# Optimization experiments

Hardware: AMD Instinct MI355X
Metric: run time of the kernel (lower is better)

## Reference

```python
import jax, jax.numpy as jnp
import numpy as np

D_MODEL = 1024
N_HEADS = 16
D_HEAD = 64
D_FF = 4096
WINDOW = 256
B, T = 2, 2048


def setup_inputs() -> dict:
    key = jax.random.key(0)
    ks = jax.random.split(key, 10)
    tot = N_HEADS * D_HEAD
    def w(k, shape):
        # approximate kaiming_normal_ fan_out init: std = sqrt(2/fan_out)
        fan_out = shape[0]
        return jax.random.normal(k, shape, jnp.float32) * np.sqrt(2.0 / fan_out)
    return {
        "x": jax.random.normal(ks[0], (B, T, D_MODEL), jnp.float32),
        "ln1_w": jnp.ones((D_MODEL,), jnp.float32),
        "qkv_w": w(ks[1], (3 * tot, D_MODEL)),
        "gate_w": w(ks[2], (tot, D_MODEL)),
        "out_w": w(ks[3], (D_MODEL, tot)),
        "ln2_w": jnp.ones((D_MODEL,), jnp.float32),
        "wg": w(ks[4], (D_FF, D_MODEL)),
        "wu": w(ks[5], (D_FF, D_MODEL)),
        "wo": w(ks[6], (D_MODEL, D_FF)),
    }


def _rmsnorm(x, w):
    return x * jax.lax.rsqrt(jnp.mean(x * x, axis=-1, keepdims=True) + 1e-6) * w


def _attention(x, qkv_w, gate_w, out_w):
    Bq, Tq, _ = x.shape
    tot = N_HEADS * D_HEAD
    qkv = x @ qkv_w.T  # [B,T,3*tot]
    q, k, v = jnp.split(qkv, 3, axis=-1)
    q = q.reshape(Bq, Tq, N_HEADS, D_HEAD).transpose(0, 2, 1, 3)
    k = k.reshape(Bq, Tq, N_HEADS, D_HEAD).transpose(0, 2, 1, 3)
    v = v.reshape(Bq, Tq, N_HEADS, D_HEAD).transpose(0, 2, 1, 3)
    scale = D_HEAD ** -0.5
    scores = jnp.einsum("bhqd,bhkd->bhqk", q, k) * scale
    pos = jnp.arange(Tq)
    dist = pos[:, None] - pos[None, :]
    allowed = (dist >= 0) & (dist < WINDOW)  # causal sliding window
    mask = jnp.where(allowed, 0.0, -jnp.inf).astype(scores.dtype)
    attn = jax.nn.softmax(scores + mask[None, None], axis=-1)
    out = jnp.einsum("bhqk,bhkd->bhqd", attn, v)
    out = out.transpose(0, 2, 1, 3).reshape(Bq, Tq, tot)
    gate = jax.nn.sigmoid(x @ gate_w.T)
    return (out * gate) @ out_w.T


def reference(x, ln1_w, qkv_w, gate_w, out_w, ln2_w, wg, wu, wo):
    x = x + _attention(_rmsnorm(x, ln1_w), qkv_w, gate_w, out_w)
    h = _rmsnorm(x, ln2_w)
    ffn = (jax.nn.silu(h @ wg.T) * (h @ wu.T)) @ wo.T
    return x + ffn
```

## Files before the change

### kernel.cpp

```cpp
#include <hip/hip_runtime.h>


#define DEV __device__ __forceinline__

using u16 = unsigned short;
typedef __attribute__((ext_vector_type(8))) short  short8;
typedef __attribute__((ext_vector_type(4))) float  floatx4;

DEV u16 f2bf(float f) {
  unsigned u = __builtin_bit_cast(unsigned, f);
  u += 0x7FFFu + ((u >> 16) & 1u);
  return (u16)(u >> 16);
}
DEV float bf2f(u16 h) {
  unsigned u = ((unsigned)h) << 16;
  return __builtin_bit_cast(float, u);
}
DEV floatx4 mfma16(short8 a, short8 b, floatx4 c) {
  return __builtin_amdgcn_mfma_f32_16x16x32_bf16(a, b, c, 0, 0, 0);
}
DEV void gload16(const u16* g, const char* lds_base_wave_uniform) {
  __builtin_amdgcn_global_load_lds(
      (const __attribute__((address_space(1))) void*)g,
      (__attribute__((address_space(3))) void*)lds_base_wave_uniform,
      16, 0, 0);
}
#define WAITVM(n) asm volatile("s_waitcnt vmcnt(" #n ")" ::: "memory")
DEV void blockbar() {
  asm volatile("" ::: "memory");
  __builtin_amdgcn_s_barrier();
  asm volatile("" ::: "memory");
}

__global__ __launch_bounds__(256) void cvt_all_k(
    const float* __restrict__ s0, const float* __restrict__ s1,
    const float* __restrict__ s2, const float* __restrict__ s3,
    const float* __restrict__ s4, const float* __restrict__ s5,
    u16* __restrict__ d0, u16* __restrict__ d1, u16* __restrict__ d2,
    u16* __restrict__ d3, u16* __restrict__ d4, u16* __restrict__ d5) {
  const int b = blockIdx.x;
  const float* in; u16* out; int base;
  if (b < 3072)       { in = s0; out = d0; base = 0; }
  else if (b < 4096)  { in = s1; out = d1; base = 3072; }
  else if (b < 5120)  { in = s2; out = d2; base = 4096; }
  else if (b < 9216)  { in = s3; out = d3; base = 5120; }
  else if (b < 13312) { in = s4; out = d4; base = 9216; }
  else                { in = s5; out = d5; base = 13312; }
  const size_t i = (size_t)(b - base) * 256 + threadIdx.x;
  const float4 v = ((const float4*)in)[i];
  ushort4 r;
  r.x = f2bf(v.x); r.y = f2bf(v.y); r.z = f2bf(v.z); r.w = f2bf(v.w);
  ((ushort4*)out)[i] = r;
}

__global__ __launch_bounds__(256) void rmsnorm_k(const float* __restrict__ x,
                                                 const float* __restrict__ wt,
                                                 u16* __restrict__ o) {
  __shared__ float red[4];
  const int row = blockIdx.x;
  const int tid = threadIdx.x;
  const float4 v = ((const float4*)(x + (size_t)row * 1024))[tid];
  float ss = v.x * v.x + v.y * v.y + v.z * v.z + v.w * v.w;
  ss += __shfl_xor(ss, 1, 64);
  ss += __shfl_xor(ss, 2, 64);
  ss += __shfl_xor(ss, 4, 64);
  ss += __shfl_xor(ss, 8, 64);
  ss += __shfl_xor(ss, 16, 64);
  ss += __shfl_xor(ss, 32, 64);
  if ((tid & 63) == 0) red[tid >> 6] = ss;
  __syncthreads();
  const float tot = red[0] + red[1] + red[2] + red[3];
  const float sc = rsqrtf(tot * (1.0f / 1024.0f) + 1e-6f);
  const float4 wv = ((const float4*)wt)[tid];
  ushort4 r;
  r.x = f2bf(v.x * sc * wv.x);
  r.y = f2bf(v.y * sc * wv.y);
  r.z = f2bf(v.z * sc * wv.z);
  r.w = f2bf(v.w * sc * wv.w);
  ((ushort4*)(o + (size_t)row * 1024))[tid] = r;
}

template <int CFG, int EPI>
__global__ __launch_bounds__(512, 2) void gemm8p(
    const u16* __restrict__ Ag, const u16* __restrict__ Bg, int N, int K,
    u16* __restrict__ cb, float* __restrict__ cf,
    const u16* __restrict__ aux, const float* __restrict__ resid,
    u16* __restrict__ cb2) {
  constexpr int BM = (CFG == 0) ? 256 : 128;
  constexpr int WM = (CFG == 0) ? 128 : 64;
  constexpr int WN = (CFG == 0) ? 64 : 32;
  constexpr int NI = WM / 16;
  constexpr int NJ = WN / 16;
  constexpr int IH = (CFG == 0) ? NI / 2 : NI;
  constexpr int GB = BM * 64;
  constexpr int QI = (CFG == 0) ? 2 : 1;
  constexpr int BUFB = 4 * GB;
  __shared__ __align__(16) char lds[2 * BUFB];

  const int tid = threadIdx.x;
  const int w = tid >> 6, lane = tid & 63;
  const int wm = w >> 2, wn = w & 3;
  const int g = lane >> 4, r16 = lane & 15;
  const int gx = (g ^ ((r16 >> 1) & 3)) << 4;

  int bid = blockIdx.y * gridDim.x + blockIdx.x;
  const int cpx = (gridDim.x * gridDim.y) >> 3;
  bid = (bid & 7) * cpx + (bid >> 3);
  const int m0 = (bid / gridDim.x) * BM;
  const int n0 = (bid % gridDim.x) * BM;

  floatx4 acc[NI][NJ];
#pragma unroll
  for (int i = 0; i < NI; i++)
#pragma unroll
    for (int j = 0; j < NJ; j++) acc[i][j] = (floatx4){0.f, 0.f, 0.f, 0.f};

  const int nt = K >> 6;

  const int kg_src = (lane & 3) ^ ((lane >> 3) & 3);
  auto stageG = [&](int G, int t) {
    if (t >= nt) return;
    const u16* Mat = (G < 2) ? Ag : Bg;
    const int b0 = (G < 2) ? m0 : n0;
    const int kc = t * 64 + (G & 1) * 32 + kg_src * 8;
    const char* dst = lds + (t & 1) * BUFB + G * GB + w * 1024;
#pragma unroll
    for (int q = 0; q < QI; q++) {
      const int row = q * 128 + w * 16 + (lane >> 2);
      gload16(Mat + (size_t)(b0 + row) * K + kc, dst + q * 8192);
    }
  };

  auto rdA = [&](short8* af, int ks, int ihalf, const char* buf) {
#pragma unroll
    for (int i = 0; i < IH; i++) {
      const int arow = wm * WM + (ihalf * IH + i) * 16 + r16;
      af[i] = *(const short8*)(buf + ks * GB + arow * 64 + gx);
    }
  };
  auto rdB = [&](short8* bf_, int ks, const char* buf) {
#pragma unroll
    for (int j = 0; j < NJ; j++) {
      const int brow = wn * WN + j * 16 + r16;
      bf_[j] = *(const short8*)(buf + 2 * GB + ks * GB + brow * 64 + gx);
    }
  };
  auto mm = [&](short8* af, short8* bf_, int ihalf) {
    __builtin_amdgcn_s_setprio(1);
#pragma unroll
    for (int i = 0; i < IH; i++)
#pragma unroll
      for (int j = 0; j < NJ; j++)
        acc[ihalf * IH + i][j] = mfma16(af[i], bf_[j], acc[ihalf * IH + i][j]);
    __builtin_amdgcn_s_setprio(0);
  };

  stageG(0, 0); stageG(2, 0); stageG(1, 0); stageG(3, 0);

  for (int t = 0; t < nt; ++t) {
    const char* buf = lds + (t & 1) * BUFB;
    short8 af[IH], bfv[NJ];
    if constexpr (CFG == 0) {
      WAITVM(4);
      blockbar();
      rdA(af, 0, 0, buf); rdB(bfv, 0, buf);
      stageG(0, t + 1);
      mm(af, bfv, 0);
      blockbar();
      rdA(af, 0, 1, buf);
      stageG(2, t + 1);
      mm(af, bfv, 1);
      if (t + 1 < nt) { WAITVM(4); } else { WAITVM(0); }
      blockbar();
      rdA(af, 1, 0, buf); rdB(bfv, 1, buf);
      stageG(1, t + 1);
      mm(af, bfv, 0);
      blockbar();
      rdA(af, 1, 1, buf);
      stageG(3, t + 1);
      mm(af, bfv, 1);
    } else {
      WAITVM(2);
      blockbar();
      rdA(af, 0, 0, buf); rdB(bfv, 0, buf);
      stageG(0, t + 1); stageG(2, t + 1);
      mm(af, bfv, 0);
      if (t + 1 < nt) { WAITVM(2); } else { WAITVM(0); }
      blockbar();
      rdA(af, 1, 0, buf); rdB(bfv, 1, buf);
      stageG(1, t + 1); stageG(3, t + 1);
      mm(af, bfv, 0);
    }
  }

#pragma unroll
  for (int i = 0; i < NI; i++) {
    const int row = m0 + wm * WM + i * 16 + g * 4;
#pragma unroll
    for (int j = 0; j < NJ; j++) {
      const int col = n0 + wn * WN + j * 16 + r16;
#pragma unroll
      for (int rr = 0; rr < 4; rr++) {
        const float v = acc[i][j][rr];
        if constexpr (EPI == 2) {
          cb[(size_t)(row + rr) * N + col] = f2bf(v / (1.0f + __expf(-v)));
        } else if constexpr (EPI == 3) {
          const size_t idx = (size_t)(row + rr) * N + col;
          cb[idx] = f2bf(v * bf2f(aux[idx]));
        } else if constexpr (EPI == 4) {
          const size_t idx = (size_t)(row + rr) * N + col;
          cf[idx] = v + resid[idx];
        } else if constexpr (EPI == 6) {
          if (col < 3072)
            cb[(size_t)(row + rr) * 3072 + col] = f2bf(v);
          else
            cb2[(size_t)(row + rr) * 1024 + (col - 3072)] =
                f2bf(1.0f / (1.0f + __expf(-v)));
        }
      }
    }
  }
}

__global__ __launch_bounds__(256) void attn_win_kernel(
    const u16* __restrict__ qkv, const u16* __restrict__ gate,
    u16* __restrict__ out) {
  __shared__ __align__(16) u16 Kl[64][80];
  __shared__ __align__(16) u16 Vt[64][80];
  __shared__ __align__(16) u16 Pl[4][16][80];

  const int tid = threadIdx.x;
  const int w = tid >> 6, lane = tid & 63;
  const int g = lane >> 4, r16 = lane & 15;

  const int q0 = blockIdx.x * 64;
  const int h = blockIdx.y;
  const int b = blockIdx.z;
  const u16* qb_ = qkv + (size_t)b * 2048 * 3072;

  const int tq = q0 + w * 16 + r16;
  const u16* qptr = qb_ + (size_t)tq * 3072 + h * 64;
  const short8 aq0 = *(const short8*)(qptr + g * 8);
  const short8 aq1 = *(const short8*)(qptr + 32 + g * 8);

  floatx4 O[4] = {{0,0,0,0},{0,0,0,0},{0,0,0,0},{0,0,0,0}};
  float mrow[4] = {-1e30f, -1e30f, -1e30f, -1e30f};
  float lrow[4] = {0.f, 0.f, 0.f, 0.f};

  const int srow = tid >> 2;
  const int sq4 = tid & 3;
  const int qw = q0 + w * 16;

  for (int kt = q0 - 256; kt <= q0; kt += 64) {
    if (kt < 0) continue;
    {
      const u16* kb = qb_ + (size_t)(kt + srow) * 3072 + 1024 + h * 64 + sq4 * 16;
      const short8 kv0 = *(const short8*)kb;
      const short8 kv1 = *(const short8*)(kb + 8);
      *(short8*)&Kl[srow][sq4 * 16] = kv0;
      *(short8*)&Kl[srow][sq4 * 16 + 8] = kv1;
      const u16* vb = kb + 1024;
      const short8 vv0 = *(const short8*)vb;
      const short8 vv1 = *(const short8*)(vb + 8);
#pragma unroll
      for (int j = 0; j < 8; j++) Vt[sq4 * 16 + j][srow] = (u16)vv0[j];
#pragma unroll
      for (int j = 0; j < 8; j++) Vt[sq4 * 16 + 8 + j][srow] = (u16)vv1[j];
    }
    __syncthreads();

    const bool active = (qw + 15 >= kt) && (qw - kt < 319);
    if (active) {
      floatx4 S[4];
#pragma unroll
      for (int nf = 0; nf < 4; nf++) {
        const short8 bk0 = *(const short8*)&Kl[nf * 16 + r16][g * 8];
        const short8 bk1 = *(const short8*)&Kl[nf * 16 + r16][32 + g * 8];
        floatx4 a = {0.f, 0.f, 0.f, 0.f};
        a = mfma16(aq0, bk0, a);
        a = mfma16(aq1, bk1, a);
        S[nf] = a;
      }
      float pm[4][4];
      float nmax[4] = {-1e30f, -1e30f, -1e30f, -1e30f};
#pragma unroll
      for (int nf = 0; nf < 4; nf++) {
        const int key = kt + nf * 16 + r16;
#pragma unroll
        for (int rr = 0; rr < 4; rr++) {
          const int q = qw + g * 4 + rr;
          const int dist = q - key;
          const float s = (dist >= 0 && dist < 256) ? S[nf][rr] : -1e30f;
          pm[nf][rr] = s;
          nmax[rr] = fmaxf(nmax[rr], s);
        }
      }
#pragma unroll
      for (int rr = 0; rr < 4; rr++) {
        float v = nmax[rr];
        v = fmaxf(v, __shfl_xor(v, 1, 64));
        v = fmaxf(v, __shfl_xor(v, 2, 64));
        v = fmaxf(v, __shfl_xor(v, 4, 64));
        v = fmaxf(v, __shfl_xor(v, 8, 64));
        const float mnew = fmaxf(mrow[rr], v);
        const float alpha = __expf(0.125f * (mrow[rr] - mnew));
        mrow[rr] = mnew;
        lrow[rr] *= alpha;
#pragma unroll
        for (int n = 0; n < 4; n++) O[n][rr] *= alpha;
        float ls = 0.f;
#pragma unroll
        for (int nf = 0; nf < 4; nf++) {
          const float s = pm[nf][rr];
          const float pv = (s < -1e29f) ? 0.f : __expf(0.125f * (s - mnew));
          pm[nf][rr] = pv;
          ls += pv;
        }
        ls += __shfl_xor(ls, 1, 64);
        ls += __shfl_xor(ls, 2, 64);
        ls += __shfl_xor(ls, 4, 64);
        ls += __shfl_xor(ls, 8, 64);
        lrow[rr] += ls;
      }
#pragma unroll
      for (int nf = 0; nf < 4; nf++)
#pragma unroll
        for (int rr = 0; rr < 4; rr++)
          Pl[w][g * 4 + rr][nf * 16 + r16] = f2bf(pm[nf][rr]);
#pragma unroll
      for (int kf = 0; kf < 2; kf++) {
        const short8 pa = *(const short8*)&Pl[w][r16][kf * 32 + g * 8];
#pragma unroll
        for (int n = 0; n < 4; n++) {
          const short8 vb8 = *(const short8*)&Vt[n * 16 + r16][kf * 32 + g * 8];
          O[n] = mfma16(pa, vb8, O[n]);
        }
      }
    }
    __syncthreads();
  }

#pragma unroll
  for (int n = 0; n < 4; n++) {
#pragma unroll
    for (int rr = 0; rr < 4; rr++) {
      const int t = qw + g * 4 + rr;
      const size_t idx = ((size_t)(b * 2048 + t)) * 1024 + h * 64 + n * 16 + r16;
      const float gv = bf2f(gate[idx]);
      const float ov = (O[n][rr] / lrow[rr]) * gv;
      out[idx] = f2bf(ov);
    }
  }
}

extern "C" void kernel_launch(void* const* d_in, const int* in_sizes, int n_in,
                              void* d_out, int out_size, void* d_ws,
                              size_t ws_size, hipStream_t stream) {
  (void)in_sizes; (void)n_in; (void)out_size; (void)ws_size;
  const float* x     = (const float*)d_in[0];
  const float* ln1   = (const float*)d_in[1];
  const float* qkvw  = (const float*)d_in[2];
  const float* gatew = (const float*)d_in[3];
  const float* outw  = (const float*)d_in[4];
  const float* ln2   = (const float*)d_in[5];
  const float* wg    = (const float*)d_in[6];
  const float* wu    = (const float*)d_in[7];
  const float* wo    = (const float*)d_in[8];
  float* outp = (float*)d_out;

  u16* p = (u16*)d_ws;
  u16* qkvw_b  = p; p += 3 * 1024 * 1024;
  u16* gatew_b = p; p += 1024 * 1024;
  u16* outw_b  = p; p += 1024 * 1024;
  u16* wg_b    = p; p += 4 * 1024 * 1024;
  u16* wu_b    = p; p += 4 * 1024 * 1024;
  u16* wo_b    = p; p += 4 * 1024 * 1024;
  u16* xn      = p; p += 4096 * 1024;
  u16* qkvb    = p; p += (size_t)4096 * 3072;
  u16* gates   = p; p += 4096 * 1024;
  u16* a3      = p; p += 4096 * 1024;
  u16* hb      = p; p += 4096 * 1024;
  u16* gs      = p; p += (size_t)4096 * 4096;
  float* x2    = (float*)p;

  cvt_all_k<<<17408, 256, 0, stream>>>(qkvw, gatew, outw, wg, wu, wo,
                                       qkvw_b, gatew_b, outw_b, wg_b, wu_b, wo_b);

  rmsnorm_k<<<4096, 256, 0, stream>>>(x, ln1, xn);

  gemm8p<0, 6><<<dim3(16, 16), 512, 0, stream>>>(
      xn, qkvw_b, 4096, 1024, qkvb, nullptr, nullptr, nullptr, gates);

  attn_win_kernel<<<dim3(32, 16, 2), 256, 0, stream>>>(qkvb, gates, a3);

  gemm8p<1, 4><<<dim3(8, 32), 512, 0, stream>>>(
      a3, outw_b, 1024, 1024, nullptr, x2, nullptr, x, nullptr);

  rmsnorm_k<<<4096, 256, 0, stream>>>(x2, ln2, hb);

  gemm8p<0, 2><<<dim3(16, 16), 512, 0, stream>>>(
      hb, wg_b, 4096, 1024, gs, nullptr, nullptr, nullptr, nullptr);
  gemm8p<0, 3><<<dim3(16, 16), 512, 0, stream>>>(
      hb, wu_b, 4096, 1024, gs, nullptr, gs, nullptr, nullptr);

  gemm8p<1, 4><<<dim3(8, 32), 512, 0, stream>>>(
      gs, wo_b, 1024, 4096, nullptr, outp, nullptr, x2, nullptr);
}
```

Measured before the change: 360.0 us.

## Split-K the FFN down-projection with large tiles and hoist A-fragment LDS reads

The final down-projection GEMM (K=4096) now runs with the larger 256x256 tile config, split four ways along K. Each split writes bf16 partial results into the reused xn/qkv workspace, and a new reduce kernel sums them and adds the residual. This trades extra memory traffic and bf16 rounding of the partial sums for better per-block compute density and shorter K loops. Separately, the CFG0 main loop now loads the second A-fragment half into its own registers before the first MFMA batch, so LDS reads overlap compute at the cost of more register pressure.

Measured after the change: 360.5 us. No clear change (+0.1%).

```diff
diff --git a/kernel.cpp b/kernel.cpp
--- a/kernel.cpp
+++ b/kernel.cpp
@@ -80,10 +80,23 @@
   ((ushort4*)(o + (size_t)row * 1024))[tid] = r;
 }
 
+__global__ __launch_bounds__(256) void reduce4_k(const u16* __restrict__ part,
+                                                 const float* __restrict__ x2,
+                                                 float* __restrict__ out) {
+  const size_t i = ((size_t)blockIdx.x * 256 + threadIdx.x) * 4;
+  float4 r = *(const float4*)(x2 + i);
+#pragma unroll
+  for (int s = 0; s < 4; s++) {
+    const ushort4 pv = *(const ushort4*)(part + (size_t)s * 4194304 + i);
+    r.x += bf2f(pv.x); r.y += bf2f(pv.y); r.z += bf2f(pv.z); r.w += bf2f(pv.w);
+  }
+  *(float4*)(out + i) = r;
+}
+
 template <int CFG, int EPI>
 __global__ __launch_bounds__(512, 2) void gemm8p(
     const u16* __restrict__ Ag, const u16* __restrict__ Bg, int N, int K,
-    u16* __restrict__ cb, float* __restrict__ cf,
+    int ksz, u16* __restrict__ cb, float* __restrict__ cf,
     const u16* __restrict__ aux, const float* __restrict__ resid,
     u16* __restrict__ cb2) {
   constexpr int BM = (CFG == 0) ? 256 : 128;
@@ -108,6 +121,7 @@
   bid = (bid & 7) * cpx + (bid >> 3);
   const int m0 = (bid / gridDim.x) * BM;
   const int n0 = (bid % gridDim.x) * BM;
+  const int kbeg = blockIdx.z * ksz;
 
   floatx4 acc[NI][NJ];
 #pragma unroll
@@ -115,14 +129,14 @@
 #pragma unroll
     for (int j = 0; j < NJ; j++) acc[i][j] = (floatx4){0.f, 0.f, 0.f, 0.f};
 
-  const int nt = K >> 6;
+  const int nt = ksz >> 6;
 
   const int kg_src = (lane & 3) ^ ((lane >> 3) & 3);
   auto stageG = [&](int G, int t) {
     if (t >= nt) return;
     const u16* Mat = (G < 2) ? Ag : Bg;
     const int b0 = (G < 2) ? m0 : n0;
-    const int kc = t * 64 + (G & 1) * 32 + kg_src * 8;
+    const int kc = kbeg + t * 64 + (G & 1) * 32 + kg_src * 8;
     const char* dst = lds + (t & 1) * BUFB + G * GB + w * 1024;
 #pragma unroll
     for (int q = 0; q < QI; q++) {
@@ -159,27 +173,28 @@
 
   for (int t = 0; t < nt; ++t) {
     const char* buf = lds + (t & 1) * BUFB;
-    short8 af[IH], bfv[NJ];
     if constexpr (CFG == 0) {
+      short8 af0[IH], af1[IH], bfv[NJ];
       WAITVM(4);
       blockbar();
-      rdA(af, 0, 0, buf); rdB(bfv, 0, buf);
+      rdA(af0, 0, 0, buf); rdB(bfv, 0, buf);
       stageG(0, t + 1);
-      mm(af, bfv, 0);
-      blockbar();
-      rdA(af, 0, 1, buf);
+      rdA(af1, 0, 1, buf);
+      mm(af0, bfv, 0);
+      blockbar();
       stageG(2, t + 1);
-      mm(af, bfv, 1);
+      mm(af1, bfv, 1);
       if (t + 1 < nt) { WAITVM(4); } else { WAITVM(0); }
       blockbar();
-      rdA(af, 1, 0, buf); rdB(bfv, 1, buf);
+      rdA(af0, 1, 0, buf); rdB(bfv, 1, buf);
       stageG(1, t + 1);
-      mm(af, bfv, 0);
-      blockbar();
-      rdA(af, 1, 1, buf);
+      rdA(af1, 1, 1, buf);
+      mm(af0, bfv, 0);
+      blockbar();
       stageG(3, t + 1);
-      mm(af, bfv, 1);
+      mm(af1, bfv, 1);
     } else {
+      short8 af[IH], bfv[NJ];
       WAITVM(2);
       blockbar();
       rdA(af, 0, 0, buf); rdB(bfv, 0, buf);
@@ -216,6 +231,9 @@
           else
             cb2[(size_t)(row + rr) * 1024 + (col - 3072)] =
                 f2bf(1.0f / (1.0f + __expf(-v)));
+        } else if constexpr (EPI == 7) {
+          (cb + (size_t)blockIdx.z * 4194304)[(size_t)(row + rr) * N + col] =
+              f2bf(v);
         }
       }
     }
@@ -382,6 +400,7 @@
   u16* hb      = p; p += 4096 * 1024;
   u16* gs      = p; p += (size_t)4096 * 4096;
   float* x2    = (float*)p;
+  u16* parts   = xn;
 
   cvt_all_k<<<17408, 256, 0, stream>>>(qkvw, gatew, outw, wg, wu, wo,
                                        qkvw_b, gatew_b, outw_b, wg_b, wu_b, wo_b);
@@ -389,20 +408,21 @@
   rmsnorm_k<<<4096, 256, 0, stream>>>(x, ln1, xn);
 
   gemm8p<0, 6><<<dim3(16, 16), 512, 0, stream>>>(
-      xn, qkvw_b, 4096, 1024, qkvb, nullptr, nullptr, nullptr, gates);
+      xn, qkvw_b, 4096, 1024, 1024, qkvb, nullptr, nullptr, nullptr, gates);
 
   attn_win_kernel<<<dim3(32, 16, 2), 256, 0, stream>>>(qkvb, gates, a3);
 
   gemm8p<1, 4><<<dim3(8, 32), 512, 0, stream>>>(
-      a3, outw_b, 1024, 1024, nullptr, x2, nullptr, x, nullptr);
+      a3, outw_b, 1024, 1024, 1024, nullptr, x2, nullptr, x, nullptr);
 
   rmsnorm_k<<<4096, 256, 0, stream>>>(x2, ln2, hb);
 
   gemm8p<0, 2><<<dim3(16, 16), 512, 0, stream>>>(
-      hb, wg_b, 4096, 1024, gs, nullptr, nullptr, nullptr, nullptr);
+      hb, wg_b, 4096, 1024, 1024, gs, nullptr, nullptr, nullptr, nullptr);
   gemm8p<0, 3><<<dim3(16, 16), 512, 0, stream>>>(
-      hb, wu_b, 4096, 1024, gs, nullptr, gs, nullptr, nullptr);
-
-  gemm8p<1, 4><<<dim3(8, 32), 512, 0, stream>>>(
-      gs, wo_b, 1024, 4096, nullptr, outp, nullptr, x2, nullptr);
-}
+      hb, wu_b, 4096, 1024, 1024, gs, nullptr, gs, nullptr, nullptr);
+
+  gemm8p<0, 7><<<dim3(4, 16, 4), 512, 0, stream>>>(
+      gs, wo_b, 1024, 4096, 1024, parts, nullptr, nullptr, nullptr, nullptr);
+  reduce4_k<<<4096, 256, 0, stream>>>(parts, x2, outp);
+}
```
